# Kernel tuning notes

Hardware: AMD Instinct MI355X
Metric: run time of the kernel (lower is better)

The kernel has to match this reference:

```python
import jax, jax.numpy as jnp
import numpy as np

B, D, H, M, N, S = 256, 256, 512, 64, 2048, 3
SHIFTS = (1, 0, -1)  # = range(S//2, -S//2, -1); matches np.roll(eye, s, axis=1) one-hot matrices


def setup_inputs():
    key = jax.random.key(0)
    k = jax.random.split(key, 24)
    f32 = jnp.float32

    def rn(i, shape, scale):
        return jax.random.normal(k[i], shape, f32) * scale

    rh = jax.random.uniform(k[3], (B, N), f32)
    wh = jax.random.uniform(k[4], (B, N), f32)
    sc_ih = 1.0 / np.sqrt(D + M)
    sc_h = 1.0 / np.sqrt(H)
    return dict(
        inp=rn(0, (B, D), 1.0),
        h_tm1=rn(1, (B, H), 0.1),
        c_tm1=rn(2, (B, H), 0.1),
        read_head_tm1=rh / rh.sum(1, keepdims=True),
        write_head_tm1=wh / wh.sum(1, keepdims=True),
        memory=rn(5, (B, N, M), 0.5),
        W_ih=rn(6, (4 * H, D + M), sc_ih), W_hh=rn(7, (4 * H, H), sc_h),
        b_ih=jnp.zeros((4 * H,), f32), b_hh=jnp.zeros((4 * H,), f32),
        W_rk=rn(8, (M, H), sc_h), b_rk=rn(9, (M,), 0.01),
        W_wk=rn(10, (M, H), sc_h), b_wk=rn(11, (M,), 0.01),
        W_rc=rn(12, (3, H), sc_h), b_rc=jnp.zeros((3,), f32),
        W_wc=rn(13, (3, H), sc_h), b_wc=jnp.zeros((3,), f32),
        W_rs=rn(14, (S, H), sc_h), b_rs=jnp.zeros((S,), f32),
        W_ws=rn(15, (S, H), sc_h), b_ws=jnp.zeros((S,), f32),
        W_w=rn(16, (2 * M, H), sc_h), b_w=jnp.zeros((2 * M,), f32),
    )


def _head_params(h, Wk, bk, Wc, bc, Ws, bs):
    kk = jnp.tanh(h @ Wk.T + bk)                     # [B,M] key
    c = h @ Wc.T + bc                                # [B,3]
    beta = jax.nn.relu(c[:, 0:1]) + 1e-4             # focus strength
    g = jax.nn.sigmoid(c[:, 1:2])                    # interpolation gate
    gamma = jax.nn.relu(c[:, 2:3]) + 1.0001          # sharpening power
    s = jax.nn.softmax(h @ Ws.T + bs, axis=1)        # [B,S] shift weights
    return kk, s, beta, g, gamma


def _address(memory, head_tm1, kk, s, beta, g, gamma):
    dot = jnp.einsum('bm,bnm->bn', kk, memory)
    nk = jnp.linalg.norm(kk, axis=1, keepdims=True)  # [B,1]
    nM = jnp.linalg.norm(memory, axis=2)             # [B,N]
    cos = dot / jnp.maximum(nk * nM, 1e-8)
    content = jax.nn.softmax(beta * cos, axis=1)
    inter = g * content + (1.0 - g) * head_tm1       # gated interpolation [B,N]
    # circular shift; identical math to contracting with the one-hot C tensor
    rolled = jnp.stack([jnp.roll(inter, -sh, axis=1) for sh in SHIFTS], axis=1)  # [B,S,N]
    out = jnp.einsum('bsn,bs->bn', rolled, s)
    out = out ** gamma                               # sharpen
    return out / out.sum(1, keepdims=True)


def reference(inp, h_tm1, c_tm1, read_head_tm1, write_head_tm1, memory,
              W_ih, W_hh, b_ih, b_hh, W_rk, b_rk, W_wk, b_wk,
              W_rc, b_rc, W_wc, b_wc, W_rs, b_rs, W_ws, b_ws, W_w, b_w):
    # read addressing uses previous hidden state
    rp = _head_params(h_tm1, W_rk, b_rk, W_rc, b_rc, W_rs, b_rs)
    read_head = _address(memory, read_head_tm1, *rp)
    M_read = jnp.einsum('bn,bnm->bm', read_head, memory)  # [B,M]
    # LSTMCell controller (torch gate order i,f,g,o)
    x = jnp.concatenate([inp, M_read], axis=1)
    z = x @ W_ih.T + b_ih + h_tm1 @ W_hh.T + b_hh
    zi, zf, zg, zo = jnp.split(z, 4, axis=1)
    c_t = jax.nn.sigmoid(zf) * c_tm1 + jax.nn.sigmoid(zi) * jnp.tanh(zg)
    h_t = jax.nn.sigmoid(zo) * jnp.tanh(c_t)
    # write addressing uses new hidden state
    wp = _head_params(h_t, W_wk, b_wk, W_wc, b_wc, W_ws, b_ws)
    write_head = _address(memory, write_head_tm1, *wp)
    wa = h_t @ W_w.T + b_w
    e = jax.nn.sigmoid(wa[:, :M])                    # erase
    a = jnp.tanh(wa[:, M:])                          # add
    ww = write_head[:, :, None]                      # [B,N,1]
    M_out = memory * (1.0 - ww * e[:, None, :]) + ww * a[:, None, :]
    return (h_t, c_t, read_head, write_head, M_out)
```

## Files before the change

### kernel.cpp

```cpp
#include <hip/hip_runtime.h>
#include <hip/hip_bf16.h>

#define Bb 256
#define Hh 512
#define Mm 64
#define Nn 2048

typedef __attribute__((ext_vector_type(8))) short bf16x8;
typedef __attribute__((ext_vector_type(4))) float f32x4;
typedef __attribute__((ext_vector_type(4))) unsigned short u16x4;
typedef __attribute__((ext_vector_type(8))) unsigned short u16x8;

static __device__ __forceinline__ short f2bf(float f) {
    unsigned u = __float_as_uint(f);
    unsigned r = (u + 0x7FFFu + ((u >> 16) & 1u)) >> 16;
    return (short)r;
}
static __device__ __forceinline__ float bf2f(unsigned short u) {
    return __uint_as_float(((unsigned)u) << 16);
}

__global__ __launch_bounds__(256) void headparams_convW_kernel(
    const float* __restrict__ h,
    const float* __restrict__ Wk, const float* __restrict__ bk,
    const float* __restrict__ Wc, const float* __restrict__ bc,
    const float* __restrict__ Ws, const float* __restrict__ bs,
    float* __restrict__ kk, float* __restrict__ par,
    const float* __restrict__ W_ih, const float* __restrict__ W_hh,
    short* __restrict__ Wb)
{
    if (blockIdx.x >= 256) {
        unsigned g = (blockIdx.x - 256) * 256 + threadIdx.x;
        unsigned j = g / 104u;
        unsigned kq = (g - j * 104u) * 8u;
        const float* src = (kq < 320u) ? (W_ih + (size_t)j * 320 + kq)
                                       : (W_hh + (size_t)j * 512 + (kq - 320u));
        float4 a = ((const float4*)src)[0];
        float4 c = ((const float4*)src)[1];
        bf16x8 o;
        o[0] = f2bf(a.x); o[1] = f2bf(a.y); o[2] = f2bf(a.z); o[3] = f2bf(a.w);
        o[4] = f2bf(c.x); o[5] = f2bf(c.y); o[6] = f2bf(c.z); o[7] = f2bf(c.w);
        *(bf16x8*)(Wb + (size_t)j * 832 + kq) = o;
        return;
    }
    int b = blockIdx.x;
    __shared__ float hs[Hh];
    __shared__ float red[6];
    __shared__ float skk[Mm];
    const float* hb = h + (size_t)b * Hh;
    for (int i = threadIdx.x; i < Hh; i += 256) hs[i] = hb[i];
    __syncthreads();
    int m = threadIdx.x >> 2, sub = threadIdx.x & 3;
    {
        const float* w = Wk + (size_t)m * Hh + sub * 128;
        const float* hh = hs + sub * 128;
        float acc = 0.f;
        #pragma unroll 8
        for (int k = 0; k < 128; ++k) acc += hh[k] * w[k];
        acc += __shfl_xor(acc, 1, 64);
        acc += __shfl_xor(acc, 2, 64);
        if (sub == 0) {
            float v = tanhf(acc + bk[m]);
            kk[(size_t)b * Mm + m] = v;
            skk[m] = v;
        }
    }
    if (threadIdx.x < 24) {
        int o = threadIdx.x >> 2, su = threadIdx.x & 3;
        const float* w = ((o < 3) ? (Wc + (size_t)o * Hh) : (Ws + (size_t)(o - 3) * Hh)) + su * 128;
        const float* hh = hs + su * 128;
        float acc = 0.f;
        #pragma unroll 8
        for (int k = 0; k < 128; ++k) acc += hh[k] * w[k];
        acc += __shfl_xor(acc, 1, 64);
        acc += __shfl_xor(acc, 2, 64);
        if (su == 0) red[o] = acc + ((o < 3) ? bc[o] : bs[o - 3]);
    }
    __syncthreads();
    if (threadIdx.x == 0) {
        float beta  = fmaxf(red[0], 0.f) + 1e-4f;
        float g     = 1.f / (1.f + __expf(-red[1]));
        float gamma = fmaxf(red[2], 0.f) + 1.0001f;
        float l0 = red[3], l1 = red[4], l2 = red[5];
        float mx = fmaxf(l0, fmaxf(l1, l2));
        float e0 = __expf(l0 - mx), e1 = __expf(l1 - mx), e2 = __expf(l2 - mx);
        float inv = 1.f / (e0 + e1 + e2);
        float ssq = 0.f;
        #pragma unroll
        for (int i = 0; i < Mm; ++i) ssq += skk[i] * skk[i];
        float* p = par + (size_t)b * 8;
        p[0] = beta; p[1] = g; p[2] = gamma;
        p[3] = e0 * inv; p[4] = e1 * inv; p[5] = e2 * inv;
        p[6] = sqrtf(ssq);
    }
}

__global__ __launch_bounds__(256) void convM_cos_kernel(
    const float* __restrict__ mem, const float* __restrict__ kk,
    const float* __restrict__ par, float* __restrict__ cosv,
    short* __restrict__ memb)
{
    int b  = blockIdx.x >> 3;
    int n0 = (blockIdx.x & 7) << 8;
    int w  = threadIdx.x >> 6;
    int l  = threadIdx.x & 63;
    int m4 = l & 15;
    int rq = l >> 4;

    float4 kv = ((const float4*)(kk + (size_t)b * Mm))[m4];
    float kn = par[(size_t)b * 8 + 6];
    const f32x4* mb4 = (const f32x4*)(mem + (size_t)b * Nn * Mm);
    short* ob = memb + (size_t)b * Nn * Mm;

    #pragma unroll
    for (int q = 0; q < 16; ++q) {
        int n = n0 + w * 64 + q * 4 + rq;
        f32x4 v = __builtin_nontemporal_load(mb4 + (size_t)n * 16 + m4);
        u16x4 o;
        o[0] = (unsigned short)f2bf(v[0]); o[1] = (unsigned short)f2bf(v[1]);
        o[2] = (unsigned short)f2bf(v[2]); o[3] = (unsigned short)f2bf(v[3]);
        *(u16x4*)(ob + (size_t)n * 64 + m4 * 4) = o;
        float dot = v[0] * kv.x + v[1] * kv.y + v[2] * kv.z + v[3] * kv.w;
        float ss  = v[0] * v[0] + v[1] * v[1] + v[2] * v[2] + v[3] * v[3];
        dot += __shfl_xor(dot, 1, 64); ss += __shfl_xor(ss, 1, 64);
        dot += __shfl_xor(dot, 2, 64); ss += __shfl_xor(ss, 2, 64);
        dot += __shfl_xor(dot, 4, 64); ss += __shfl_xor(ss, 4, 64);
        dot += __shfl_xor(dot, 8, 64); ss += __shfl_xor(ss, 8, 64);
        if (m4 == 0) cosv[(size_t)b * Nn + n] = dot / fmaxf(kn * sqrtf(ss), 1e-8f);
    }
}

__global__ __launch_bounds__(1024) void raddr_mread_convA_kernel(
    const float* __restrict__ cosv, const float* __restrict__ par,
    const float* __restrict__ prev, const short* __restrict__ memb,
    const float* __restrict__ inp, const float* __restrict__ h,
    float* __restrict__ outh, short* __restrict__ Ab)
{
    int b = blockIdx.x;
    int t = threadIdx.x;
    int w = t >> 6, l = t & 63;
    __shared__ float csh[Nn];
    __shared__ float redw[16];
    __shared__ float redM[128][8][8];
    __shared__ float mrdL[Mm];

    const float* pv = par + (size_t)b * 8;
    float beta = pv[0], g = pv[1], gamma = pv[2];
    float s0 = pv[3], s1 = pv[4], s2 = pv[5];

    float v0 = beta * cosv[(size_t)b * Nn + t];
    float v1 = beta * cosv[(size_t)b * Nn + t + 1024];
    float mx = fmaxf(v0, v1);
    #pragma unroll
    for (int msk = 1; msk < 64; msk <<= 1) mx = fmaxf(mx, __shfl_xor(mx, msk, 64));
    if (l == 0) redw[w] = mx;
    __syncthreads();
    mx = redw[0];
    #pragma unroll
    for (int i = 1; i < 16; ++i) mx = fmaxf(mx, redw[i]);
    float e0 = __expf(v0 - mx), e1 = __expf(v1 - mx);
    float sum = e0 + e1;
    #pragma unroll
    for (int msk = 1; msk < 64; msk <<= 1) sum += __shfl_xor(sum, msk, 64);
    __syncthreads();
    if (l == 0) redw[w] = sum;
    __syncthreads();
    sum = 0.f;
    #pragma unroll
    for (int i = 0; i < 16; ++i) sum += redw[i];
    float invs = 1.f / sum;
    const float* pb = prev + (size_t)b * Nn;
    float i0 = g * e0 * invs + (1.f - g) * pb[t];
    float i1 = g * e1 * invs + (1.f - g) * pb[t + 1024];
    csh[t] = i0; csh[t + 1024] = i1;
    __syncthreads();
    int n1 = t + 1024;
    float c0 = s0 * csh[(t + 1) & (Nn - 1)] + s1 * i0 + s2 * csh[(t - 1) & (Nn - 1)];
    float c1 = s0 * csh[(n1 + 1) & (Nn - 1)] + s1 * i1 + s2 * csh[(n1 - 1) & (Nn - 1)];
    float p0 = exp2f(gamma * __log2f(c0));
    float p1 = exp2f(gamma * __log2f(c1));
    float osum = p0 + p1;
    #pragma unroll
    for (int msk = 1; msk < 64; msk <<= 1) osum += __shfl_xor(osum, msk, 64);
    __syncthreads();
    if (l == 0) redw[w] = osum;
    __syncthreads();
    osum = 0.f;
    #pragma unroll
    for (int i = 0; i < 16; ++i) osum += redw[i];
    float inv2 = 1.f / osum;
    float h0 = p0 * inv2, h1 = p1 * inv2;
    outh[(size_t)b * Nn + t] = h0;
    outh[(size_t)b * Nn + n1] = h1;
    __syncthreads();
    csh[t] = h0; csh[n1] = h1;
    __syncthreads();

    int m8 = t & 7;
    int r  = t >> 3;
    const short* mb = memb + (size_t)b * Nn * Mm;
    u16x8 uv[16];
    float wg[16];
    #pragma unroll
    for (int it = 0; it < 16; ++it) {
        int n = it * 128 + r;
        uv[it] = *(const u16x8*)(mb + (size_t)n * 64 + m8 * 8);
        wg[it] = csh[n];
    }
    float acc[8] = {};
    #pragma unroll
    for (int it = 0; it < 16; ++it) {
        #pragma unroll
        for (int j = 0; j < 8; ++j) acc[j] += wg[it] * bf2f(uv[it][j]);
    }
    #pragma unroll
    for (int j = 0; j < 8; ++j) redM[r][m8][j] = acc[j];
    __syncthreads();
    if (t < 64) {
        int mm8 = t >> 3, j = t & 7;
        float s = 0.f;
        #pragma unroll 16
        for (int r2 = 0; r2 < 128; ++r2) s += redM[r2][mm8][j];
        mrdL[mm8 * 8 + j] = s;
    }
    __syncthreads();

    if (t < 104) {
        int kq = t * 8;
        float v[8];
        if (kq < 256) {
            const float* s = inp + (size_t)b * 256 + kq;
            #pragma unroll
            for (int i = 0; i < 8; ++i) v[i] = s[i];
        } else if (kq < 320) {
            #pragma unroll
            for (int i = 0; i < 8; ++i) v[i] = mrdL[kq - 256 + i];
        } else {
            const float* s = h + (size_t)b * 512 + (kq - 320);
            #pragma unroll
            for (int i = 0; i < 8; ++i) v[i] = s[i];
        }
        bf16x8 o;
        #pragma unroll
        for (int i = 0; i < 8; ++i) o[i] = f2bf(v[i]);
        *(bf16x8*)(Ab + (size_t)b * 832 + kq) = o;
    }
}

__global__ __launch_bounds__(256) void lstm_gemm_mfma(
    const short* __restrict__ Ab, const short* __restrict__ Wb,
    const float* __restrict__ b_ih, const float* __restrict__ b_hh,
    float* __restrict__ z)
{
    int t = threadIdx.x;
    int r0 = blockIdx.x * 64, c0 = blockIdx.y * 64;
    int w = t >> 6, l = t & 63;
    int wr = (w >> 1) * 32, wc = (w & 1) * 32;
    int lr = l & 15, kb = (l >> 4) * 8;

    const short* A0 = Ab + (size_t)(r0 + wr + lr) * 832 + kb;
    const short* A1 = A0 + 16 * 832;
    const short* B0 = Wb + (size_t)(c0 + wc + lr) * 832 + kb;
    const short* B1 = B0 + 16 * 832;

    f32x4 acc00 = {0.f, 0.f, 0.f, 0.f}, acc01 = {0.f, 0.f, 0.f, 0.f};
    f32x4 acc10 = {0.f, 0.f, 0.f, 0.f}, acc11 = {0.f, 0.f, 0.f, 0.f};

    #pragma unroll 2
    for (int kt = 0; kt < 26; ++kt) {
        int k0 = kt * 32;
        bf16x8 a0 = *(const bf16x8*)(A0 + k0);
        bf16x8 a1 = *(const bf16x8*)(A1 + k0);
        bf16x8 b0 = *(const bf16x8*)(B0 + k0);
        bf16x8 b1 = *(const bf16x8*)(B1 + k0);
        acc00 = __builtin_amdgcn_mfma_f32_16x16x32_bf16(a0, b0, acc00, 0, 0, 0);
        acc01 = __builtin_amdgcn_mfma_f32_16x16x32_bf16(a0, b1, acc01, 0, 0, 0);
        acc10 = __builtin_amdgcn_mfma_f32_16x16x32_bf16(a1, b0, acc10, 0, 0, 0);
        acc11 = __builtin_amdgcn_mfma_f32_16x16x32_bf16(a1, b1, acc11, 0, 0, 0);
    }
    int rq = (l >> 4) * 4;
    #pragma unroll
    for (int q = 0; q < 4; ++q) {
        int row0 = r0 + wr + rq + q;
        int col0 = c0 + wc + lr;
        z[(size_t)row0 * 2048 + col0] = acc00[q] + b_ih[col0] + b_hh[col0];
        z[(size_t)row0 * 2048 + col0 + 16] = acc01[q] + b_ih[col0 + 16] + b_hh[col0 + 16];
        z[(size_t)(row0 + 16) * 2048 + col0] = acc10[q] + b_ih[col0] + b_hh[col0];
        z[(size_t)(row0 + 16) * 2048 + col0 + 16] = acc11[q] + b_ih[col0 + 16] + b_hh[col0 + 16];
    }
}

__global__ __launch_bounds__(1024) void gates_wfused_kernel(
    const float* __restrict__ z, const float* __restrict__ c_tm1,
    const float* __restrict__ Wk, const float* __restrict__ bk,
    const float* __restrict__ Wc, const float* __restrict__ bc,
    const float* __restrict__ Ws, const float* __restrict__ bs,
    const float* __restrict__ W_w, const float* __restrict__ b_w,
    const short* __restrict__ memb, const float* __restrict__ prev,
    float* __restrict__ h_out, float* __restrict__ c_out,
    float* __restrict__ ea, float* __restrict__ outh)
{
    int b = blockIdx.x;
    int t = threadIdx.x;
    int w = t >> 6, l = t & 63;
    __shared__ float hs[Hh];
    __shared__ float red6[6];
    __shared__ float skk[Mm];
    __shared__ float parL[8];
    __shared__ float csh[Nn];
    __shared__ float redw[16];

    if (t < 512) {
        const float* zb = z + (size_t)b * 2048;
        float zi = zb[t], zf = zb[512 + t], zg = zb[1024 + t], zo = zb[1536 + t];
        float si = 1.f / (1.f + __expf(-zi));
        float sf = 1.f / (1.f + __expf(-zf));
        float so = 1.f / (1.f + __expf(-zo));
        float ct = sf * c_tm1[(size_t)b * 512 + t] + si * tanhf(zg);
        float ht = so * tanhf(ct);
        c_out[(size_t)b * 512 + t] = ct;
        h_out[(size_t)b * 512 + t] = ht;
        hs[t] = ht;
    }
    __syncthreads();

    if (t < 256) {
        int m = t >> 2, sub = t & 3;
        const float* wv = Wk + (size_t)m * Hh + sub * 128;
        const float* hh = hs + sub * 128;
        float acc = 0.f;
        #pragma unroll 8
        for (int k = 0; k < 128; ++k) acc += hh[k] * wv[k];
        acc += __shfl_xor(acc, 1, 64);
        acc += __shfl_xor(acc, 2, 64);
        if (sub == 0) skk[m] = tanhf(acc + bk[m]);
    } else if (t < 280) {
        int o = (t - 256) >> 2, su = t & 3;
        const float* wv = ((o < 3) ? (Wc + (size_t)o * Hh) : (Ws + (size_t)(o - 3) * Hh)) + su * 128;
        const float* hh = hs + su * 128;
        float acc = 0.f;
        #pragma unroll 8
        for (int k = 0; k < 128; ++k) acc += hh[k] * wv[k];
        acc += __shfl_xor(acc, 1, 64);
        acc += __shfl_xor(acc, 2, 64);
        if (su == 0) red6[o] = acc + ((o < 3) ? bc[o] : bs[o - 3]);
    } else if (t >= 512) {
        int o = (t - 512) >> 2, su = t & 3;
        const float* wv = W_w + (size_t)o * Hh + su * 128;
        const float* hh = hs + su * 128;
        float acc = 0.f;
        #pragma unroll 8
        for (int k = 0; k < 128; ++k) acc += hh[k] * wv[k];
        acc += __shfl_xor(acc, 1, 64);
        acc += __shfl_xor(acc, 2, 64);
        if (su == 0) {
            float v = acc + b_w[o];
            ea[(size_t)b * 128 + o] = (o < Mm) ? (1.f / (1.f + __expf(-v))) : tanhf(v);
        }
    }
    __syncthreads();
    if (t < 64) {
        float v = skk[t];
        float ssq = v * v;
        #pragma unroll
        for (int msk = 1; msk < 64; msk <<= 1) ssq += __shfl_xor(ssq, msk, 64);
        if (t == 0) {
            parL[6] = sqrtf(ssq);
            parL[0] = fmaxf(red6[0], 0.f) + 1e-4f;
            parL[1] = 1.f / (1.f + __expf(-red6[1]));
            parL[2] = fmaxf(red6[2], 0.f) + 1.0001f;
            float l0 = red6[3], l1 = red6[4], l2 = red6[5];
            float mx = fmaxf(l0, fmaxf(l1, l2));
            float e0 = __expf(l0 - mx), e1 = __expf(l1 - mx), e2 = __expf(l2 - mx);
            float inv = 1.f / (e0 + e1 + e2);
            parL[3] = e0 * inv; parL[4] = e1 * inv; parL[5] = e2 * inv;
        }
    }
    __syncthreads();

    {
        int m8 = l & 7, rg = l >> 3;
        float kv8[8];
        #pragma unroll
        for (int j = 0; j < 8; ++j) kv8[j] = skk[m8 * 8 + j];
        float kn = parL[6];
        const short* mb = memb + (size_t)b * Nn * Mm;
        u16x8 uv[16];
        #pragma unroll
        for (int it = 0; it < 16; ++it) {
            int n = it * 128 + w * 8 + rg;
            uv[it] = *(const u16x8*)(mb + (size_t)n * 64 + m8 * 8);
        }
        #pragma unroll
        for (int it = 0; it < 16; ++it) {
            int n = it * 128 + w * 8 + rg;
            float dot = 0.f, ss = 0.f;
            #pragma unroll
            for (int j = 0; j < 8; ++j) {
                float x = bf2f(uv[it][j]);
                dot += x * kv8[j];
                ss  += x * x;
            }
            dot += __shfl_xor(dot, 1, 64); ss += __shfl_xor(ss, 1, 64);
            dot += __shfl_xor(dot, 2, 64); ss += __shfl_xor(ss, 2, 64);
            dot += __shfl_xor(dot, 4, 64); ss += __shfl_xor(ss, 4, 64);
            if (m8 == 0) csh[n] = dot / fmaxf(kn * sqrtf(ss), 1e-8f);
        }
    }
    __syncthreads();

    {
        float beta = parL[0], g = parL[1], gamma = parL[2];
        float s0 = parL[3], s1 = parL[4], s2 = parL[5];
        float v0 = beta * csh[t], v1 = beta * csh[t + 1024];
        float mx = fmaxf(v0, v1);
        #pragma unroll
        for (int msk = 1; msk < 64; msk <<= 1) mx = fmaxf(mx, __shfl_xor(mx, msk, 64));
        if (l == 0) redw[w] = mx;
        __syncthreads();
        mx = redw[0];
        #pragma unroll
        for (int i = 1; i < 16; ++i) mx = fmaxf(mx, redw[i]);
        float e0 = __expf(v0 - mx), e1 = __expf(v1 - mx);
        float sum = e0 + e1;
        #pragma unroll
        for (int msk = 1; msk < 64; msk <<= 1) sum += __shfl_xor(sum, msk, 64);
        __syncthreads();
        if (l == 0) redw[w] = sum;
        __syncthreads();
        sum = 0.f;
        #pragma unroll
        for (int i = 0; i < 16; ++i) sum += redw[i];
        float invs = 1.f / sum;
        const float* pb = prev + (size_t)b * Nn;
        float i0 = g * e0 * invs + (1.f - g) * pb[t];
        float i1 = g * e1 * invs + (1.f - g) * pb[t + 1024];
        __syncthreads();
        csh[t] = i0; csh[t + 1024] = i1;
        __syncthreads();
        int n1 = t + 1024;
        float c0 = s0 * csh[(t + 1) & (Nn - 1)] + s1 * i0 + s2 * csh[(t - 1) & (Nn - 1)];
        float c1 = s0 * csh[(n1 + 1) & (Nn - 1)] + s1 * i1 + s2 * csh[(n1 - 1) & (Nn - 1)];
        float p0 = exp2f(gamma * __log2f(c0));
        float p1 = exp2f(gamma * __log2f(c1));
        float osum = p0 + p1;
        #pragma unroll
        for (int msk = 1; msk < 64; msk <<= 1) osum += __shfl_xor(osum, msk, 64);
        __syncthreads();
        if (l == 0) redw[w] = osum;
        __syncthreads();
        osum = 0.f;
        #pragma unroll
        for (int i = 0; i < 16; ++i) osum += redw[i];
        float inv2 = 1.f / osum;
        outh[(size_t)b * Nn + t] = p0 * inv2;
        outh[(size_t)b * Nn + n1] = p1 * inv2;
    }
}

template <int BF16SRC>
__global__ __launch_bounds__(256) void mout_kernel(
    const float* __restrict__ mem, const short* __restrict__ memb,
    const float* __restrict__ head, const float* __restrict__ ea,
    float* __restrict__ out)
{
    const size_t total8 = (size_t)Bb * Nn * Mm / 8;
    for (size_t i8 = (size_t)blockIdx.x * 256 + threadIdx.x; i8 < total8;
         i8 += (size_t)2048 * 256) {
        size_t row = i8 >> 3;
        int m8 = (int)(i8 & 7);
        int b = (int)(row >> 11);
        float w = head[row];
        float x[8];
        if (BF16SRC) {
            u16x8 uv = __builtin_nontemporal_load((const u16x8*)memb + i8);
            #pragma unroll
            for (int j = 0; j < 8; ++j) x[j] = bf2f(uv[j]);
        } else {
            f32x4 lo = __builtin_nontemporal_load((const f32x4*)mem + i8 * 2);
            f32x4 hi = __builtin_nontemporal_load((const f32x4*)mem + i8 * 2 + 1);
            #pragma unroll
            for (int j = 0; j < 4; ++j) { x[j] = lo[j]; x[4 + j] = hi[j]; }
        }
        const float* ep = ea + (size_t)b * 128 + m8 * 8;
        const float* ap = ep + 64;
        f32x4 o0, o1;
        #pragma unroll
        for (int j = 0; j < 4; ++j) {
            o0[j] = x[j] * (1.f - w * ep[j]) + w * ap[j];
            o1[j] = x[4 + j] * (1.f - w * ep[4 + j]) + w * ap[4 + j];
        }
        __builtin_nontemporal_store(o0, (f32x4*)out + i8 * 2);
        __builtin_nontemporal_store(o1, (f32x4*)out + i8 * 2 + 1);
    }
}

extern "C" void kernel_launch(void* const* d_in, const int* in_sizes, int n_in,
                              void* d_out, int out_size, void* d_ws, size_t ws_size,
                              hipStream_t stream)
{
    const float* inp   = (const float*)d_in[0];
    const float* h_tm1 = (const float*)d_in[1];
    const float* c_tm1 = (const float*)d_in[2];
    const float* rh0   = (const float*)d_in[3];
    const float* wh0   = (const float*)d_in[4];
    const float* mem   = (const float*)d_in[5];
    const float* W_ih  = (const float*)d_in[6];
    const float* W_hh  = (const float*)d_in[7];
    const float* b_ih  = (const float*)d_in[8];
    const float* b_hh  = (const float*)d_in[9];
    const float* W_rk  = (const float*)d_in[10];
    const float* b_rk  = (const float*)d_in[11];
    const float* W_wk  = (const float*)d_in[12];
    const float* b_wk  = (const float*)d_in[13];
    const float* W_rc  = (const float*)d_in[14];
    const float* b_rc  = (const float*)d_in[15];
    const float* W_wc  = (const float*)d_in[16];
    const float* b_wc  = (const float*)d_in[17];
    const float* W_rs  = (const float*)d_in[18];
    const float* b_rs  = (const float*)d_in[19];
    const float* W_ws  = (const float*)d_in[20];
    const float* b_ws  = (const float*)d_in[21];
    const float* W_w   = (const float*)d_in[22];
    const float* b_w   = (const float*)d_in[23];

    float* out   = (float*)d_out;
    float* h_t   = out;
    float* c_t   = out + 131072;
    float* rhead = out + 262144;
    float* whead = out + 786432;
    float* mo    = out + 1310720;
    float* cosbuf = mo;
    float* zbuf   = mo + 524288;
    short* Ab     = (short*)(mo + 1048576);
    short* Wb     = (short*)(mo + 1179648);

    float* ws  = (float*)d_ws;
    float* kk  = ws;
    float* par = ws + 16384;
    float* ea  = ws + 18432;

    const size_t memb_elems = (size_t)Bb * Nn * Mm;
    const bool big_ws = ws_size >= (size_t)51200 * 4 + memb_elems * 2;
    short* memb = big_ws ? (short*)(ws + 51200)
                         : (short*)(mo + 2097152);

    headparams_convW_kernel<<<1088, 256, 0, stream>>>(
        h_tm1, W_rk, b_rk, W_rc, b_rc, W_rs, b_rs, kk, par, W_ih, W_hh, Wb);
    convM_cos_kernel<<<2048, 256, 0, stream>>>(mem, kk, par, cosbuf, memb);
    raddr_mread_convA_kernel<<<Bb, 1024, 0, stream>>>(
        cosbuf, par, rh0, memb, inp, h_tm1, rhead, Ab);
    lstm_gemm_mfma<<<dim3(4, 32), 256, 0, stream>>>(Ab, Wb, b_ih, b_hh, zbuf);
    gates_wfused_kernel<<<Bb, 1024, 0, stream>>>(
        zbuf, c_tm1, W_wk, b_wk, W_wc, b_wc, W_ws, b_ws, W_w, b_w,
        memb, wh0, h_t, c_t, ea, whead);
    if (big_ws)
        mout_kernel<1><<<2048, 256, 0, stream>>>(mem, memb, whead, ea, mo);
    else
        mout_kernel<0><<<2048, 256, 0, stream>>>(mem, memb, whead, ea, mo);
}
```

Measured before the change: 158.3 us.

## Split fused per-batch address kernels into wider-grid memory passes

New measurement: 160.4 us. About the same (+1.3%).

```diff
diff --git a/kernel.cpp b/kernel.cpp
--- a/kernel.cpp
+++ b/kernel.cpp
@@ -130,19 +130,15 @@
     }
 }
 
-__global__ __launch_bounds__(1024) void raddr_mread_convA_kernel(
+__global__ __launch_bounds__(1024) void address_kernel(
     const float* __restrict__ cosv, const float* __restrict__ par,
-    const float* __restrict__ prev, const short* __restrict__ memb,
-    const float* __restrict__ inp, const float* __restrict__ h,
-    float* __restrict__ outh, short* __restrict__ Ab)
+    const float* __restrict__ prev, float* __restrict__ outh)
 {
     int b = blockIdx.x;
     int t = threadIdx.x;
     int w = t >> 6, l = t & 63;
     __shared__ float csh[Nn];
     __shared__ float redw[16];
-    __shared__ float redM[128][8][8];
-    __shared__ float mrdL[Mm];
 
     const float* pv = par + (size_t)b * 8;
     float beta = pv[0], g = pv[1], gamma = pv[2];
@@ -189,42 +185,54 @@
     #pragma unroll
     for (int i = 0; i < 16; ++i) osum += redw[i];
     float inv2 = 1.f / osum;
-    float h0 = p0 * inv2, h1 = p1 * inv2;
-    outh[(size_t)b * Nn + t] = h0;
-    outh[(size_t)b * Nn + n1] = h1;
-    __syncthreads();
-    csh[t] = h0; csh[n1] = h1;
-    __syncthreads();
-
-    int m8 = t & 7;
-    int r  = t >> 3;
+    outh[(size_t)b * Nn + t] = p0 * inv2;
+    outh[(size_t)b * Nn + n1] = p1 * inv2;
+}
+
+__global__ __launch_bounds__(256) void mread_partial_kernel(
+    const short* __restrict__ memb, const float* __restrict__ rhead,
+    float* __restrict__ psc)
+{
+    int b = blockIdx.x >> 3, ch = blockIdx.x & 7;
+    int t = threadIdx.x;
+    int m8 = t & 7, r = t >> 3;
     const short* mb = memb + (size_t)b * Nn * Mm;
-    u16x8 uv[16];
-    float wg[16];
-    #pragma unroll
-    for (int it = 0; it < 16; ++it) {
-        int n = it * 128 + r;
-        uv[it] = *(const u16x8*)(mb + (size_t)n * 64 + m8 * 8);
-        wg[it] = csh[n];
-    }
+    const float* hb = rhead + (size_t)b * Nn;
     float acc[8] = {};
     #pragma unroll
-    for (int it = 0; it < 16; ++it) {
-        #pragma unroll
-        for (int j = 0; j < 8; ++j) acc[j] += wg[it] * bf2f(uv[it][j]);
-    }
-    #pragma unroll
-    for (int j = 0; j < 8; ++j) redM[r][m8][j] = acc[j];
+    for (int it = 0; it < 8; ++it) {
+        int n = ch * 256 + it * 32 + r;
+        float wgt = hb[n];
+        u16x8 uv = *(const u16x8*)(mb + (size_t)n * 64 + m8 * 8);
+        #pragma unroll
+        for (int j = 0; j < 8; ++j) acc[j] += wgt * bf2f(uv[j]);
+    }
+    __shared__ float red[32][64];
+    #pragma unroll
+    for (int j = 0; j < 8; ++j) red[r][m8 * 8 + j] = acc[j];
     __syncthreads();
     if (t < 64) {
-        int mm8 = t >> 3, j = t & 7;
         float s = 0.f;
-        #pragma unroll 16
-        for (int r2 = 0; r2 < 128; ++r2) s += redM[r2][mm8][j];
-        mrdL[mm8 * 8 + j] = s;
-    }
-    __syncthreads();
-
+        #pragma unroll
+        for (int rr = 0; rr < 32; ++rr) s += red[rr][t];
+        psc[((size_t)b * 8 + ch) * 64 + t] = s;
+    }
+}
+
+__global__ __launch_bounds__(128) void convA_kernel(
+    const float* __restrict__ psc, const float* __restrict__ inp,
+    const float* __restrict__ h, short* __restrict__ Ab)
+{
+    int b = blockIdx.x;
+    int t = threadIdx.x;
+    __shared__ float mrdL[Mm];
+    if (t < 64) {
+        float s = 0.f;
+        #pragma unroll
+        for (int ch = 0; ch < 8; ++ch) s += psc[((size_t)b * 8 + ch) * 64 + t];
+        mrdL[t] = s;
+    }
+    __syncthreads();
     if (t < 104) {
         int kq = t * 8;
         float v[8];
@@ -290,25 +298,20 @@
     }
 }
 
-__global__ __launch_bounds__(1024) void gates_wfused_kernel(
+__global__ __launch_bounds__(1024) void gates_wparams_kernel(
     const float* __restrict__ z, const float* __restrict__ c_tm1,
     const float* __restrict__ Wk, const float* __restrict__ bk,
     const float* __restrict__ Wc, const float* __restrict__ bc,
     const float* __restrict__ Ws, const float* __restrict__ bs,
     const float* __restrict__ W_w, const float* __restrict__ b_w,
-    const short* __restrict__ memb, const float* __restrict__ prev,
     float* __restrict__ h_out, float* __restrict__ c_out,
-    float* __restrict__ ea, float* __restrict__ outh)
+    float* __restrict__ kk, float* __restrict__ par, float* __restrict__ ea)
 {
     int b = blockIdx.x;
     int t = threadIdx.x;
-    int w = t >> 6, l = t & 63;
     __shared__ float hs[Hh];
     __shared__ float red6[6];
     __shared__ float skk[Mm];
-    __shared__ float parL[8];
-    __shared__ float csh[Nn];
-    __shared__ float redw[16];
 
     if (t < 512) {
         const float* zb = z + (size_t)b * 2048;
@@ -333,7 +336,11 @@
         for (int k = 0; k < 128; ++k) acc += hh[k] * wv[k];
         acc += __shfl_xor(acc, 1, 64);
         acc += __shfl_xor(acc, 2, 64);
-        if (sub == 0) skk[m] = tanhf(acc + bk[m]);
+        if (sub == 0) {
+            float v = tanhf(acc + bk[m]);
+            skk[m] = v;
+            kk[(size_t)b * Mm + m] = v;
+        }
     } else if (t < 280) {
         int o = (t - 256) >> 2, su = t & 3;
         const float* wv = ((o < 3) ? (Wc + (size_t)o * Hh) : (Ws + (size_t)(o - 3) * Hh)) + su * 128;
@@ -365,96 +372,50 @@
         #pragma unroll
         for (int msk = 1; msk < 64; msk <<= 1) ssq += __shfl_xor(ssq, msk, 64);
         if (t == 0) {
-            parL[6] = sqrtf(ssq);
-            parL[0] = fmaxf(red6[0], 0.f) + 1e-4f;
-            parL[1] = 1.f / (1.f + __expf(-red6[1]));
-            parL[2] = fmaxf(red6[2], 0.f) + 1.0001f;
+            float* p = par + (size_t)b * 8;
+            p[6] = sqrtf(ssq);
+            p[0] = fmaxf(red6[0], 0.f) + 1e-4f;
+            p[1] = 1.f / (1.f + __expf(-red6[1]));
+            p[2] = fmaxf(red6[2], 0.f) + 1.0001f;
             float l0 = red6[3], l1 = red6[4], l2 = red6[5];
             float mx = fmaxf(l0, fmaxf(l1, l2));
             float e0 = __expf(l0 - mx), e1 = __expf(l1 - mx), e2 = __expf(l2 - mx);
             float inv = 1.f / (e0 + e1 + e2);
-            parL[3] = e0 * inv; parL[4] = e1 * inv; parL[5] = e2 * inv;
-        }
-    }
-    __syncthreads();
-
+            p[3] = e0 * inv; p[4] = e1 * inv; p[5] = e2 * inv;
+        }
+    }
+}
+
+__global__ __launch_bounds__(256) void wcos_kernel(
+    const short* __restrict__ memb, const float* __restrict__ kk,
+    const float* __restrict__ par, float* __restrict__ cosv)
+{
+    int b = blockIdx.x >> 3, ch = blockIdx.x & 7;
+    int w = threadIdx.x >> 6, l = threadIdx.x & 63;
+    int m8 = l & 7, rg = l >> 3;
+    float kv8[8];
     {
-        int m8 = l & 7, rg = l >> 3;
-        float kv8[8];
-        #pragma unroll
-        for (int j = 0; j < 8; ++j) kv8[j] = skk[m8 * 8 + j];
-        float kn = parL[6];
-        const short* mb = memb + (size_t)b * Nn * Mm;
-        u16x8 uv[16];
-        #pragma unroll
-        for (int it = 0; it < 16; ++it) {
-            int n = it * 128 + w * 8 + rg;
-            uv[it] = *(const u16x8*)(mb + (size_t)n * 64 + m8 * 8);
-        }
-        #pragma unroll
-        for (int it = 0; it < 16; ++it) {
-            int n = it * 128 + w * 8 + rg;
-            float dot = 0.f, ss = 0.f;
-            #pragma unroll
-            for (int j = 0; j < 8; ++j) {
-                float x = bf2f(uv[it][j]);
-                dot += x * kv8[j];
-                ss  += x * x;
-            }
-            dot += __shfl_xor(dot, 1, 64); ss += __shfl_xor(ss, 1, 64);
-            dot += __shfl_xor(dot, 2, 64); ss += __shfl_xor(ss, 2, 64);
-            dot += __shfl_xor(dot, 4, 64); ss += __shfl_xor(ss, 4, 64);
-            if (m8 == 0) csh[n] = dot / fmaxf(kn * sqrtf(ss), 1e-8f);
-        }
-    }
-    __syncthreads();
-
-    {
-        float beta = parL[0], g = parL[1], gamma = parL[2];
-        float s0 = parL[3], s1 = parL[4], s2 = parL[5];
-        float v0 = beta * csh[t], v1 = beta * csh[t + 1024];
-        float mx = fmaxf(v0, v1);
-        #pragma unroll
-        for (int msk = 1; msk < 64; msk <<= 1) mx = fmaxf(mx, __shfl_xor(mx, msk, 64));
-        if (l == 0) redw[w] = mx;
-        __syncthreads();
-        mx = redw[0];
-        #pragma unroll
-        for (int i = 1; i < 16; ++i) mx = fmaxf(mx, redw[i]);
-        float e0 = __expf(v0 - mx), e1 = __expf(v1 - mx);
-        float sum = e0 + e1;
-        #pragma unroll
-        for (int msk = 1; msk < 64; msk <<= 1) sum += __shfl_xor(sum, msk, 64);
-        __syncthreads();
-        if (l == 0) redw[w] = sum;
-        __syncthreads();
-        sum = 0.f;
-        #pragma unroll
-        for (int i = 0; i < 16; ++i) sum += redw[i];
-        float invs = 1.f / sum;
-        const float* pb = prev + (size_t)b * Nn;
-        float i0 = g * e0 * invs + (1.f - g) * pb[t];
-        float i1 = g * e1 * invs + (1.f - g) * pb[t + 1024];
-        __syncthreads();
-        csh[t] = i0; csh[t + 1024] = i1;
-        __syncthreads();
-        int n1 = t + 1024;
-        float c0 = s0 * csh[(t + 1) & (Nn - 1)] + s1 * i0 + s2 * csh[(t - 1) & (Nn - 1)];
-        float c1 = s0 * csh[(n1 + 1) & (Nn - 1)] + s1 * i1 + s2 * csh[(n1 - 1) & (Nn - 1)];
-        float p0 = exp2f(gamma * __log2f(c0));
-        float p1 = exp2f(gamma * __log2f(c1));
-        float osum = p0 + p1;
-        #pragma unroll
-        for (int msk = 1; msk < 64; msk <<= 1) osum += __shfl_xor(osum, msk, 64);
-        __syncthreads();
-        if (l == 0) redw[w] = osum;
-        __syncthreads();
-        osum = 0.f;
-        #pragma unroll
-        for (int i = 0; i < 16; ++i) osum += redw[i];
-        float inv2 = 1.f / osum;
-        outh[(size_t)b * Nn + t] = p0 * inv2;
-        outh[(size_t)b * Nn + n1] = p1 * inv2;
+        const float* kp = kk + (size_t)b * Mm + m8 * 8;
+        #pragma unroll
+        for (int j = 0; j < 8; ++j) kv8[j] = kp[j];
+    }
+    float kn = par[(size_t)b * 8 + 6];
+    const short* mb = memb + (size_t)b * Nn * Mm;
+    #pragma unroll
+    for (int it = 0; it < 8; ++it) {
+        int n = ch * 256 + it * 32 + w * 8 + rg;
+        u16x8 uv = *(const u16x8*)(mb + (size_t)n * 64 + m8 * 8);
+        float dot = 0.f, ss = 0.f;
+        #pragma unroll
+        for (int j = 0; j < 8; ++j) {
+            float x = bf2f(uv[j]);
+            dot += x * kv8[j];
+            ss  += x * x;
+        }
+        dot += __shfl_xor(dot, 1, 64); ss += __shfl_xor(ss, 1, 64);
+        dot += __shfl_xor(dot, 2, 64); ss += __shfl_xor(ss, 2, 64);
+        dot += __shfl_xor(dot, 4, 64); ss += __shfl_xor(ss, 4, 64);
+        if (m8 == 0) cosv[(size_t)b * Nn + n] = dot / fmaxf(kn * sqrtf(ss), 1e-8f);
     }
 }
 
@@ -544,16 +505,20 @@
     const bool big_ws = ws_size >= (size_t)51200 * 4 + memb_elems * 2;
     short* memb = big_ws ? (short*)(ws + 51200)
                          : (short*)(mo + 2097152);
+    float* psc  = mo + 18874368;
 
     headparams_convW_kernel<<<1088, 256, 0, stream>>>(
         h_tm1, W_rk, b_rk, W_rc, b_rc, W_rs, b_rs, kk, par, W_ih, W_hh, Wb);
     convM_cos_kernel<<<2048, 256, 0, stream>>>(mem, kk, par, cosbuf, memb);
-    raddr_mread_convA_kernel<<<Bb, 1024, 0, stream>>>(
-        cosbuf, par, rh0, memb, inp, h_tm1, rhead, Ab);
+    address_kernel<<<Bb, 1024, 0, stream>>>(cosbuf, par, rh0, rhead);
+    mread_partial_kernel<<<2048, 256, 0, stream>>>(memb, rhead, psc);
+    convA_kernel<<<Bb, 128, 0, stream>>>(psc, inp, h_tm1, Ab);
     lstm_gemm_mfma<<<dim3(4, 32), 256, 0, stream>>>(Ab, Wb, b_ih, b_hh, zbuf);
-    gates_wfused_kernel<<<Bb, 1024, 0, stream>>>(
+    gates_wparams_kernel<<<Bb, 1024, 0, stream>>>(
         zbuf, c_tm1, W_wk, b_wk, W_wc, b_wc, W_ws, b_ws, W_w, b_w,
-        memb, wh0, h_t, c_t, ea, whead);
+        h_t, c_t, kk, par, ea);
+    wcos_kernel<<<2048, 256, 0, stream>>>(memb, kk, par, cosbuf);
+    address_kernel<<<Bb, 1024, 0, stream>>>(cosbuf, par, wh0, whead);
     if (big_ws)
         mout_kernel<1><<<2048, 256, 0, stream>>>(mem, memb, whead, ea, mo);
     else
```
